# Performance work log

Measured on AMD Instinct MI355X. Metric: run time of the kernel, lower is better.

The kernel has to match this reference:

```python
import jax, jax.numpy as jnp
import numpy as np

N, E, G = 50000, 500000, 64
IN_F, H_F, HEADS, OUT_F = 128, 64, 4, 326000
NEG_SLOPE = 0.2


def _gat_layer(h, W, a_src, a_dst, b, src, dst):
    # h: [N, H_F]; W: [H_F, HEADS*H_F]; a_src/a_dst: [HEADS, H_F]; b: [H_F]
    x = (h @ W).reshape(N, HEADS, H_F)                      # per-head transform
    ls = jnp.einsum('nhc,hc->nh', x, a_src)                  # [N, HEADS]
    ld = jnp.einsum('nhc,hc->nh', x, a_dst)
    e = jax.nn.leaky_relu(ls[src] + ld[dst], NEG_SLOPE)      # [E', HEADS] edge logits
    m = jax.ops.segment_max(e, dst, num_segments=N)          # segment-softmax (stable)
    m = jnp.where(jnp.isfinite(m), m, 0.0)
    ex = jnp.exp(e - m[dst])
    denom = jax.ops.segment_sum(ex, dst, num_segments=N)
    alpha = ex / (denom[dst] + 1e-16)                        # [E', HEADS]
    out = jax.ops.segment_sum(x[src] * alpha[:, :, None], dst, num_segments=N)  # [N,HEADS,H_F]
    return out.mean(axis=1) + b                              # concat=False -> head mean + bias


def setup_inputs() -> dict:
    key = jax.random.key(0)
    ks = jax.random.split(key, 24)
    inp = {
        'x': jax.random.normal(ks[0], (N, IN_F), dtype=jnp.float32),
        'edge_index': jax.random.randint(ks[1], (2, E), 0, N, dtype=jnp.int32),
        'edge_attr': jax.random.normal(ks[2], (E, 16), dtype=jnp.float32),
        'batch': jnp.sort(jax.random.randint(ks[3], (N,), 0, G, dtype=jnp.int32)),
        'W_emb': jax.random.normal(ks[4], (IN_F, H_F), dtype=jnp.float32) * 0.05,
        'b_emb': jnp.zeros((H_F,), dtype=jnp.float32),
        'W_fc': jax.random.normal(ks[5], (H_F, OUT_F), dtype=jnp.float32) * 0.05,
        'b_fc': jnp.zeros((OUT_F,), dtype=jnp.float32),
    }
    for l in range(3):
        inp[f'W{l+1}'] = jax.random.normal(ks[6 + 4 * l], (H_F, HEADS * H_F), dtype=jnp.float32) * 0.05
        inp[f'a_src{l+1}'] = jax.random.normal(ks[7 + 4 * l], (HEADS, H_F), dtype=jnp.float32) * 0.1
        inp[f'a_dst{l+1}'] = jax.random.normal(ks[8 + 4 * l], (HEADS, H_F), dtype=jnp.float32) * 0.1
        inp[f'b{l+1}'] = jnp.zeros((H_F,), dtype=jnp.float32)
    return inp


def reference(x, edge_index, edge_attr, batch, W_emb, b_emb,
              W1, a_src1, a_dst1, b1, W2, a_src2, a_dst2, b2,
              W3, a_src3, a_dst3, b3, W_fc, b_fc):
    # add self loops (PyG GATConv default)
    loop = jnp.arange(N, dtype=edge_index.dtype)
    src = jnp.concatenate([edge_index[0], loop])
    dst = jnp.concatenate([edge_index[1], loop])

    h = x @ W_emb + b_emb
    for (W, a_s, a_d, b) in ((W1, a_src1, a_dst1, b1), (W2, a_src2, a_dst2, b2), (W3, a_src3, a_dst3, b3)):
        h = jax.nn.relu(_gat_layer(h, W, a_s, a_d, b, src, dst))

    # global mean pool over graphs
    sums = jax.ops.segment_sum(h, batch, num_segments=G)
    cnt = jax.ops.segment_sum(jnp.ones((N,), h.dtype), batch, num_segments=G)
    pooled = sums / jnp.maximum(cnt, 1.0)[:, None]
    # dropout is identity in eval mode
    return pooled @ W_fc + b_fc
```

## Files before the change

kernel.cpp:

```cpp
#include <hip/hip_runtime.h>

#define NN 50000
#define EE 500000
#define GG 64
#define IN_F 128
#define H_F 64
#define HEADS 4
#define OUT_F 326000
#define NEG 0.2f
#define SCAN_B 256
#define NBLK ((NN + SCAN_B - 1) / SCAN_B)

__global__ __launch_bounds__(256) void k_emb(const float* __restrict__ x,
                                             const float* __restrict__ Wemb,
                                             const float* __restrict__ bemb,
                                             float* __restrict__ h0) {
    __shared__ float wlds[IN_F * H_F];
    int t = threadIdx.x;
#pragma unroll
    for (int i = 0; i < (IN_F * H_F) / (4 * 256); ++i)
        ((float4*)wlds)[t + 256 * i] = ((const float4*)Wemb)[t + 256 * i];
    __syncthreads();

    int c = t & 63, sub = t >> 6;
    int n0 = __builtin_amdgcn_readfirstlane(blockIdx.x * 32 + sub * 8);
    float bv = bemb[c];

    if (n0 + 8 <= NN) {
        const float4* xr = (const float4*)(x + (size_t)n0 * IN_F);
        float acc[8] = {0.f, 0.f, 0.f, 0.f, 0.f, 0.f, 0.f, 0.f};
        for (int k4 = 0; k4 < IN_F / 4; ++k4) {
            float w0 = wlds[(4 * k4 + 0) * H_F + c];
            float w1 = wlds[(4 * k4 + 1) * H_F + c];
            float w2 = wlds[(4 * k4 + 2) * H_F + c];
            float w3 = wlds[(4 * k4 + 3) * H_F + c];
#pragma unroll
            for (int j = 0; j < 8; ++j) {
                float4 xv = xr[j * (IN_F / 4) + k4];
                acc[j] = fmaf(xv.x, w0,
                         fmaf(xv.y, w1,
                         fmaf(xv.z, w2,
                         fmaf(xv.w, w3, acc[j]))));
            }
        }
#pragma unroll
        for (int j = 0; j < 8; ++j)
            h0[(size_t)(n0 + j) * H_F + c] = acc[j] + bv;
    } else {
        for (int j = 0; j < 8; ++j) {
            int n = n0 + j;
            if (n >= NN) break;
            const float* xrow = x + (size_t)n * IN_F;
            float a = 0.f;
            for (int k = 0; k < IN_F; ++k) a += xrow[k] * wlds[k * H_F + c];
            h0[(size_t)n * H_F + c] = a + bv;
        }
    }
}

__global__ __launch_bounds__(256) void k_gemm_layer(const float* __restrict__ h,
                                                    const float* __restrict__ W,
                                                    const float* __restrict__ a_src,
                                                    const float* __restrict__ a_dst,
                                                    float* __restrict__ xbuf,
                                                    float* __restrict__ ls,
                                                    float* __restrict__ ld) {
    __shared__ float tb[2][2][256];
    int t = threadIdx.x;
    int lane = t & 63, wv = t >> 6;
    float wreg[H_F];
#pragma unroll
    for (int k = 0; k < H_F; ++k) wreg[k] = W[k * (HEADS * H_F) + t];
    float asv = a_src[t], adv = a_dst[t];
    int base = blockIdx.x * 32;
    int rdi = (t & 3) * 64 + (t >> 2);
    for (int i = 0; i < 32; i += 2) {
        int n0 = base + i;
        if (n0 >= NN) break;
        int n1 = n0 + 1;
        const float* h0r = h + (size_t)n0 * H_F;
        const float* h1r = h + (size_t)n1 * H_F;
        float a0 = 0.f, a1 = 0.f, b0 = 0.f, b1 = 0.f;
#pragma unroll
        for (int k = 0; k < H_F; k += 2) {
            a0 = fmaf(h0r[k], wreg[k], a0);
            a1 = fmaf(h0r[k + 1], wreg[k + 1], a1);
            b0 = fmaf(h1r[k], wreg[k], b0);
            b1 = fmaf(h1r[k + 1], wreg[k + 1], b1);
        }
        float acc0 = a0 + a1, acc1 = b0 + b1;
        int p = (i >> 1) & 1;
        tb[p][0][t] = acc0;
        tb[p][1][t] = acc1;
#pragma unroll
        for (int rep = 0; rep < 2; ++rep) {
            float acc = rep ? acc1 : acc0;
            int n = rep ? n1 : n0;
            float vs = acc * asv, vd = acc * adv;
#pragma unroll
            for (int off = 32; off; off >>= 1) {
                vs += __shfl_xor(vs, off, 64);
                vd += __shfl_xor(vd, off, 64);
            }
            if (lane == 0) {
                ls[n * HEADS + wv] = vs;
                ld[n * HEADS + wv] = vd;
            }
        }
        __syncthreads();
        xbuf[(size_t)n0 * (HEADS * H_F) + t] = tb[p][0][rdi];
        xbuf[(size_t)n1 * (HEADS * H_F) + t] = tb[p][1][rdi];
    }
}

__device__ __forceinline__ float lrelu_exp(float e) {
    e = (e > 0.f) ? e : NEG * e;
    return __expf(e);
}

__device__ __forceinline__ float4 lexp4(float4 s, float4 d) {
    float4 r;
    r.x = lrelu_exp(s.x + d.x);
    r.y = lrelu_exp(s.y + d.y);
    r.z = lrelu_exp(s.z + d.z);
    r.w = lrelu_exp(s.w + d.w);
    return r;
}

__global__ void k_count(const int* __restrict__ dst, int* __restrict__ cnt) {
    int i = blockIdx.x * blockDim.x + threadIdx.x;
    if (i >= EE + NN) return;
    int d = (i < EE) ? dst[i] : (i - EE);
    atomicAdd(&cnt[d], 1);
}

__global__ void k_scan1(const int* __restrict__ cnt, int* __restrict__ excl,
                        int* __restrict__ bsum) {
    __shared__ int lds[SCAN_B];
    int t = threadIdx.x, i = blockIdx.x * SCAN_B + t;
    int v = (i < NN) ? cnt[i] : 0;
    lds[t] = v;
    __syncthreads();
    for (int off = 1; off < SCAN_B; off <<= 1) {
        int add = (t >= off) ? lds[t - off] : 0;
        __syncthreads();
        lds[t] += add;
        __syncthreads();
    }
    if (i < NN) excl[i] = lds[t] - v;
    if (t == SCAN_B - 1) bsum[blockIdx.x] = lds[t];
}

__global__ void k_scan2(int* __restrict__ bsum) {
    __shared__ int lds[SCAN_B];
    int t = threadIdx.x;
    int v = (t < NBLK) ? bsum[t] : 0;
    lds[t] = v;
    __syncthreads();
    for (int off = 1; off < SCAN_B; off <<= 1) {
        int add = (t >= off) ? lds[t - off] : 0;
        __syncthreads();
        lds[t] += add;
        __syncthreads();
    }
    if (t < NBLK) bsum[t] = lds[t] - v;
}

__global__ void k_scan3(const int* __restrict__ excl, const int* __restrict__ bsum,
                        int* __restrict__ row, int* __restrict__ cursor) {
    int i = blockIdx.x * blockDim.x + threadIdx.x;
    if (i >= NN) return;
    int r = excl[i] + bsum[i / SCAN_B];
    row[i] = r;
    cursor[i] = r;
    if (i == 0) row[NN] = EE + NN;
}

__global__ void k_scatter(const int* __restrict__ src, const int* __restrict__ dst,
                          int* __restrict__ cursor, int* __restrict__ csr_src) {
    int i = blockIdx.x * blockDim.x + threadIdx.x;
    if (i >= EE + NN) return;
    int s, d;
    if (i < EE) { s = src[i]; d = dst[i]; } else { s = d = i - EE; }
    int pos = atomicAdd(&cursor[d], 1);
    csr_src[pos] = s;
}

__global__ __launch_bounds__(256) void k_aggr_csr(const int* __restrict__ row,
                                                  const int* __restrict__ csr_src,
                                                  const float4* __restrict__ ls4,
                                                  const float4* __restrict__ ld4,
                                                  const float4* __restrict__ xb4,
                                                  const float* __restrict__ bias,
                                                  float* __restrict__ hout) {
    int t = threadIdx.x;
    int lane = t & 63, wv = t >> 6;
    int dA = blockIdx.x * 8 + wv * 2;
    int dB = dA + 1;
    if (dA >= NN) return;
    int r0A = row[dA], r1A = row[dA + 1];
    int r0B = row[dB], r1B = row[dB + 1];
    float4 bldA = ld4[dA];
    float4 bldB = ld4[dB];
    float4 accA = {0.f, 0.f, 0.f, 0.f}, denA = {1e-16f, 1e-16f, 1e-16f, 1e-16f};
    float4 accB = {0.f, 0.f, 0.f, 0.f}, denB = {1e-16f, 1e-16f, 1e-16f, 1e-16f};

    int jA = r0A, jB = r0B;
    int sA = (jA < r1A) ? csr_src[jA] : 0;
    int sB = (jB < r1B) ? csr_src[jB] : 0;

    while (jA < r1A && jB < r1B) {
        int sa = __builtin_amdgcn_readfirstlane(sA);
        int sb = __builtin_amdgcn_readfirstlane(sB);
        float4 xa = xb4[(size_t)sa * H_F + lane];
        float4 xb = xb4[(size_t)sb * H_F + lane];
        float4 la = ls4[sa];
        float4 lb = ls4[sb];
        ++jA; if (jA < r1A) sA = csr_src[jA];
        ++jB; if (jB < r1B) sB = csr_src[jB];
        float4 ea = lexp4(la, bldA);
        float4 eb = lexp4(lb, bldB);
        denA.x += ea.x; denA.y += ea.y; denA.z += ea.z; denA.w += ea.w;
        denB.x += eb.x; denB.y += eb.y; denB.z += eb.z; denB.w += eb.w;
        accA.x = fmaf(ea.x, xa.x, accA.x);
        accA.y = fmaf(ea.y, xa.y, accA.y);
        accA.z = fmaf(ea.z, xa.z, accA.z);
        accA.w = fmaf(ea.w, xa.w, accA.w);
        accB.x = fmaf(eb.x, xb.x, accB.x);
        accB.y = fmaf(eb.y, xb.y, accB.y);
        accB.z = fmaf(eb.z, xb.z, accB.z);
        accB.w = fmaf(eb.w, xb.w, accB.w);
    }
    while (jA < r1A) {
        int sa = __builtin_amdgcn_readfirstlane(sA);
        float4 xa = xb4[(size_t)sa * H_F + lane];
        float4 la = ls4[sa];
        ++jA; if (jA < r1A) sA = csr_src[jA];
        float4 ea = lexp4(la, bldA);
        denA.x += ea.x; denA.y += ea.y; denA.z += ea.z; denA.w += ea.w;
        accA.x = fmaf(ea.x, xa.x, accA.x);
        accA.y = fmaf(ea.y, xa.y, accA.y);
        accA.z = fmaf(ea.z, xa.z, accA.z);
        accA.w = fmaf(ea.w, xa.w, accA.w);
    }
    while (jB < r1B) {
        int sb = __builtin_amdgcn_readfirstlane(sB);
        float4 xb = xb4[(size_t)sb * H_F + lane];
        float4 lb = ls4[sb];
        ++jB; if (jB < r1B) sB = csr_src[jB];
        float4 eb = lexp4(lb, bldB);
        denB.x += eb.x; denB.y += eb.y; denB.z += eb.z; denB.w += eb.w;
        accB.x = fmaf(eb.x, xb.x, accB.x);
        accB.y = fmaf(eb.y, xb.y, accB.y);
        accB.z = fmaf(eb.z, xb.z, accB.z);
        accB.w = fmaf(eb.w, xb.w, accB.w);
    }

    float bv = bias[lane];
    float resA = 0.25f * (accA.x / denA.x + accA.y / denA.y +
                          accA.z / denA.z + accA.w / denA.w);
    float resB = 0.25f * (accB.x / denB.x + accB.y / denB.y +
                          accB.z / denB.z + accB.w / denB.w);
    hout[(size_t)dA * H_F + lane] = fmaxf(resA + bv, 0.f);
    hout[(size_t)dB * H_F + lane] = fmaxf(resB + bv, 0.f);
}

__global__ void k_starts(const int* __restrict__ batch, int* __restrict__ starts) {
    int g = threadIdx.x;
    if (g > GG) return;
    int lo = 0, hi = NN;
    while (lo < hi) {
        int mid = (lo + hi) >> 1;
        if (batch[mid] < g) lo = mid + 1; else hi = mid;
    }
    starts[g] = lo;
}

__global__ void k_pool(const float* __restrict__ h, const int* __restrict__ starts,
                       float* __restrict__ pooledT) {
    int g = blockIdx.x;
    int s = starts[g], e = starts[g + 1];
    int t = threadIdx.x;
    int c = t & 63, j = t >> 6;
    float sum = 0.f;
    for (int n = s + j; n < e; n += 4) sum += h[(size_t)n * H_F + c];
    __shared__ float lds[256];
    lds[t] = sum;
    __syncthreads();
    if (j == 0) {
        float tot = lds[c] + lds[64 + c] + lds[128 + c] + lds[192 + c];
        int cnt = e - s;
        float inv = 1.0f / (float)(cnt > 0 ? cnt : 1);
        pooledT[c * GG + g] = tot * inv;
    }
}

__global__ __launch_bounds__(256) void k_fc(const float* __restrict__ pooledT,
                                            const float* __restrict__ Wfc,
                                            const float* __restrict__ bfc,
                                            float* __restrict__ out) {
    int o = blockIdx.x * blockDim.x + threadIdx.x;
    if (o >= OUT_F) return;
    float acc[GG];
#pragma unroll
    for (int g = 0; g < GG; ++g) acc[g] = 0.f;
    for (int c = 0; c < H_F; ++c) {
        float w = Wfc[(size_t)c * OUT_F + o];
        const float4* pr4 = (const float4*)(pooledT + c * GG);
#pragma unroll
        for (int g4 = 0; g4 < GG / 4; ++g4) {
            float4 p = pr4[g4];
            acc[4 * g4 + 0] = fmaf(p.x, w, acc[4 * g4 + 0]);
            acc[4 * g4 + 1] = fmaf(p.y, w, acc[4 * g4 + 1]);
            acc[4 * g4 + 2] = fmaf(p.z, w, acc[4 * g4 + 2]);
            acc[4 * g4 + 3] = fmaf(p.w, w, acc[4 * g4 + 3]);
        }
    }
    float bv = bfc[o];
    for (int g = 0; g < GG; ++g) out[(size_t)g * OUT_F + o] = acc[g] + bv;
}

extern "C" void kernel_launch(void* const* d_in, const int* in_sizes, int n_in,
                              void* d_out, int out_size, void* d_ws, size_t ws_size,
                              hipStream_t stream) {
    const float* x      = (const float*)d_in[0];
    const int*   eidx   = (const int*)d_in[1];
    const int*   batch  = (const int*)d_in[3];
    const float* W_emb  = (const float*)d_in[4];
    const float* b_emb  = (const float*)d_in[5];
    const float* W_fc   = (const float*)d_in[6];
    const float* b_fc   = (const float*)d_in[7];
    const float* Wl[3]   = {(const float*)d_in[8],  (const float*)d_in[12], (const float*)d_in[16]};
    const float* asl[3]  = {(const float*)d_in[9],  (const float*)d_in[13], (const float*)d_in[17]};
    const float* adl[3]  = {(const float*)d_in[10], (const float*)d_in[14], (const float*)d_in[18]};
    const float* bl[3]   = {(const float*)d_in[11], (const float*)d_in[15], (const float*)d_in[19]};

    const int* src = eidx;
    const int* dst = eidx + EE;

    float* xbuf    = (float*)d_ws;
    float* hA      = xbuf + (size_t)NN * 256;
    float* hB      = hA + (size_t)NN * 64;
    float* ls      = hB + (size_t)NN * 64;
    float* ldb     = ls + (size_t)NN * 4;
    float* pooledT = ldb + (size_t)NN * 4;
    int*   starts  = (int*)(pooledT + GG * GG);
    int*   cnt     = starts + 128;
    int*   excl    = cnt + NN;
    int*   bsum    = excl + NN;
    int*   row     = bsum + 256;
    int*   cursor  = row + NN + 4;
    int*   csr_src = cursor + NN;

    hipMemsetAsync(cnt, 0, (size_t)NN * sizeof(int), stream);
    k_count<<<(EE + NN + 255) / 256, 256, 0, stream>>>(dst, cnt);
    k_scan1<<<NBLK, SCAN_B, 0, stream>>>(cnt, excl, bsum);
    k_scan2<<<1, SCAN_B, 0, stream>>>(bsum);
    k_scan3<<<(NN + 255) / 256, 256, 0, stream>>>(excl, bsum, row, cursor);
    k_scatter<<<(EE + NN + 255) / 256, 256, 0, stream>>>(src, dst, cursor, csr_src);

    k_emb<<<(NN + 31) / 32, 256, 0, stream>>>(x, W_emb, b_emb, hA);

    float* hcur = hA;
    float* hnext = hB;
    for (int l = 0; l < 3; ++l) {
        k_gemm_layer<<<(NN + 31) / 32, 256, 0, stream>>>(hcur, Wl[l], asl[l], adl[l],
                                                         xbuf, ls, ldb);
        k_aggr_csr<<<NN / 8, 256, 0, stream>>>(row, csr_src,
                                               (const float4*)ls, (const float4*)ldb,
                                               (const float4*)xbuf, bl[l], hnext);
        float* tmp = hcur; hcur = hnext; hnext = tmp;
    }

    k_starts<<<1, 128, 0, stream>>>(batch, starts);
    k_pool<<<GG, 256, 0, stream>>>(hcur, starts, pooledT);
    k_fc<<<(OUT_F + 255) / 256, 256, 0, stream>>>(pooledT, W_fc, b_fc, (float*)d_out);
}
```

Baseline: 1.018 ms.

## Restructure per-layer GEMM to stage weight half in LDS and compute 8 rows per thread

The per-layer transform kernel now splits heads across two blocks, stages each block's half of W in shared memory, and has each thread accumulate 8 node rows using float4 loads of h with wave-uniform row addresses. This replaces the per-thread 64-register weight copy and the shared-memory transpose plus barrier per row pair. The aim is more register reuse and fewer barriers, at the cost of twice as many blocks, scattered strided xbuf stores, and the 8-row inner loop skipping a bounds check for the tail.

```diff
diff --git a/kernel.cpp b/kernel.cpp
--- a/kernel.cpp
+++ b/kernel.cpp
@@ -65,51 +65,64 @@
                                                     float* __restrict__ xbuf,
                                                     float* __restrict__ ls,
                                                     float* __restrict__ ld) {
-    __shared__ float tb[2][2][256];
-    int t = threadIdx.x;
-    int lane = t & 63, wv = t >> 6;
-    float wreg[H_F];
-#pragma unroll
-    for (int k = 0; k < H_F; ++k) wreg[k] = W[k * (HEADS * H_F) + t];
-    float asv = a_src[t], adv = a_dst[t];
-    int base = blockIdx.x * 32;
-    int rdi = (t & 3) * 64 + (t >> 2);
-    for (int i = 0; i < 32; i += 2) {
-        int n0 = base + i;
+    __shared__ float wlds[H_F * 128];
+    int t = threadIdx.x;
+    int hp = blockIdx.x & 1;
+    int nbase = (blockIdx.x >> 1) * 32;
+    {
+        const float4* W4 = (const float4*)W;
+        float4* wl4 = (float4*)wlds;
+#pragma unroll
+        for (int i = 0; i < 8; ++i) {
+            int flat = t + 256 * i;
+            int k = flat >> 5;
+            int off = flat & 31;
+            wl4[flat] = W4[k * 64 + hp * 32 + off];
+        }
+    }
+    int lane = t & 63;
+    int hd2 = (t >> 6) & 1;
+    int q = t >> 7;
+    int hd = hp * 2 + hd2;
+    float asv = a_src[hd * 64 + lane];
+    float adv = a_dst[hd * 64 + lane];
+    __syncthreads();
+
+    const float* wcol = wlds + hd2 * 64 + lane;
+    for (int g = 0; g < 2; ++g) {
+        int n0 = __builtin_amdgcn_readfirstlane(nbase + q * 16 + g * 8);
         if (n0 >= NN) break;
-        int n1 = n0 + 1;
-        const float* h0r = h + (size_t)n0 * H_F;
-        const float* h1r = h + (size_t)n1 * H_F;
-        float a0 = 0.f, a1 = 0.f, b0 = 0.f, b1 = 0.f;
-#pragma unroll
-        for (int k = 0; k < H_F; k += 2) {
-            a0 = fmaf(h0r[k], wreg[k], a0);
-            a1 = fmaf(h0r[k + 1], wreg[k + 1], a1);
-            b0 = fmaf(h1r[k], wreg[k], b0);
-            b1 = fmaf(h1r[k + 1], wreg[k + 1], b1);
-        }
-        float acc0 = a0 + a1, acc1 = b0 + b1;
-        int p = (i >> 1) & 1;
-        tb[p][0][t] = acc0;
-        tb[p][1][t] = acc1;
-#pragma unroll
-        for (int rep = 0; rep < 2; ++rep) {
-            float acc = rep ? acc1 : acc0;
-            int n = rep ? n1 : n0;
-            float vs = acc * asv, vd = acc * adv;
+        const float4* hr = (const float4*)(h + (size_t)n0 * H_F);
+        float acc[8] = {0.f, 0.f, 0.f, 0.f, 0.f, 0.f, 0.f, 0.f};
+        for (int k4 = 0; k4 < H_F / 4; ++k4) {
+            float w0 = wcol[(4 * k4 + 0) * 128];
+            float w1 = wcol[(4 * k4 + 1) * 128];
+            float w2 = wcol[(4 * k4 + 2) * 128];
+            float w3 = wcol[(4 * k4 + 3) * 128];
+#pragma unroll
+            for (int j = 0; j < 8; ++j) {
+                float4 hv = hr[j * (H_F / 4) + k4];
+                acc[j] = fmaf(hv.x, w0,
+                         fmaf(hv.y, w1,
+                         fmaf(hv.z, w2,
+                         fmaf(hv.w, w3, acc[j]))));
+            }
+        }
+#pragma unroll
+        for (int j = 0; j < 8; ++j) {
+            int n = n0 + j;
+            xbuf[(size_t)n * (HEADS * H_F) + lane * 4 + hd] = acc[j];
+            float vs = acc[j] * asv, vd = acc[j] * adv;
 #pragma unroll
             for (int off = 32; off; off >>= 1) {
                 vs += __shfl_xor(vs, off, 64);
                 vd += __shfl_xor(vd, off, 64);
             }
             if (lane == 0) {
-                ls[n * HEADS + wv] = vs;
-                ld[n * HEADS + wv] = vd;
+                ls[n * HEADS + hd] = vs;
+                ld[n * HEADS + hd] = vd;
             }
         }
-        __syncthreads();
-        xbuf[(size_t)n0 * (HEADS * H_F) + t] = tb[p][0][rdi];
-        xbuf[(size_t)n1 * (HEADS * H_F) + t] = tb[p][1][rdi];
     }
 }
 
@@ -364,8 +377,8 @@
     float* hcur = hA;
     float* hnext = hB;
     for (int l = 0; l < 3; ++l) {
-        k_gemm_layer<<<(NN + 31) / 32, 256, 0, stream>>>(hcur, Wl[l], asl[l], adl[l],
-                                                         xbuf, ls, ldb);
+        k_gemm_layer<<<2 * ((NN + 31) / 32), 256, 0, stream>>>(hcur, Wl[l], asl[l], adl[l],
+                                                               xbuf, ls, ldb);
         k_aggr_csr<<<NN / 8, 256, 0, stream>>>(row, csr_src,
                                                (const float4*)ls, (const float4*)ldb,
                                                (const float4*)xbuf, bl[l], hnext);
```

New measurement: 979.0 us. 1.04x faster.
